# Kernel optimization log

Measured on AMD Instinct MI355X. Metric: run time of the kernel, lower is better.

## Reference

```python
import jax, jax.numpy as jnp
import numpy as np
import math

FACTOR = 5  # self.factor


def setup_inputs() -> dict:
    key = jax.random.key(0)
    kq, kk, kv = jax.random.split(key, 3)
    B, L, H, D = 4, 2048, 8, 64
    return {
        "queries": jax.random.normal(kq, (B, L, H, D), dtype=jnp.float32),
        "keys": jax.random.normal(kk, (B, L, H, D), dtype=jnp.float32),
        "values": jax.random.normal(kv, (B, L, H, D), dtype=jnp.float32),
        "attn_mask": jnp.zeros((1,), dtype=jnp.int32),  # unused by the module's forward
    }


def _prob_attention(queries, keys, values):
    B, L_Q, H, D = queries.shape
    L_K = keys.shape[1]
    # to (B, H, L, D)
    Q = queries.transpose(0, 2, 1, 3)
    K = keys.transpose(0, 2, 1, 3)
    V = values.transpose(0, 2, 1, 3)

    U_part = min(FACTOR * int(math.ceil(math.log(L_K))), L_K)  # sample_k
    u = min(FACTOR * int(math.ceil(math.log(L_Q))), L_Q)       # n_top

    # --- _prob_QE: sampled QK, sparsity measure M, top-u query selection ---
    idx_key = jax.random.key(42)  # fixed key stands in for torch.randint
    index_sample = jax.random.randint(idx_key, (L_Q, U_part), 0, L_K)  # [L_Q, S]
    K_sample = K[:, :, index_sample, :]                                # [B,H,L_Q,S,E]
    Q_K_sample = jnp.einsum('bhqe,bhqse->bhqs', Q, K_sample)           # [B,H,L_Q,S]
    M = Q_K_sample.max(axis=-1) - Q_K_sample.sum(axis=-1) / L_K        # [B,H,L_Q]
    M_top = jax.lax.top_k(M, u)[1]                                     # [B,H,u]

    Q_reduce = jnp.take_along_axis(Q, M_top[..., None], axis=2)        # [B,H,u,E]
    scores = jnp.einsum('bhue,bhke->bhuk', Q_reduce, K)                # [B,H,u,L_K]
    scores = scores * (1.0 / math.sqrt(D))                             # scale=None -> 1/sqrt(D)

    # --- initial context (mask_flag=True path): mean of V over keys ---
    context = jnp.broadcast_to(V.mean(axis=2, keepdims=True), (B, H, L_Q, D))

    attn = jax.nn.softmax(scores, axis=-1)
    context_update = jnp.einsum('bhuk,bhkd->bhud', attn, V)            # [B,H,u,D]

    # scatter the updated rows back at the selected query positions
    b = jnp.arange(B)[:, None, None]
    h = jnp.arange(H)[None, :, None]
    context = context.at[b, h, M_top].set(context_update)

    return context.transpose(0, 2, 1, 3)  # [B, L_Q, H, D]


def reference(queries, keys, values, attn_mask):
    # attn_mask is accepted but unused by the torch module's mask_flag=True path
    return _prob_attention(queries, keys, values)
```

## Files before the change

kernel.cpp:

```cpp
#include <hip/hip_runtime.h>
#include <stdint.h>


static constexpr int Bc = 4, Lc = 2048, Hc = 8, Dc = 64, NUc = 40;
static constexpr int NCH = 32, CHK = 64;
static constexpr int UT = 10;

struct TF2 { uint32_t a, b; };

__host__ __device__ constexpr uint32_t rotl32c(uint32_t x, int r) {
    return (x << r) | (x >> (32 - r));
}

__host__ __device__ constexpr TF2 tf2x32c(uint32_t k0, uint32_t k1, uint32_t x0, uint32_t x1) {
    uint32_t ks[3] = {k0, k1, k0 ^ k1 ^ 0x1BD11BDAu};
    const int R0[4] = {13, 15, 26, 6};
    const int R1[4] = {17, 29, 16, 24};
    x0 += ks[0];
    x1 += ks[1];
    for (int i = 0; i < 5; ++i) {
        const int* R = (i & 1) ? R1 : R0;
        for (int j = 0; j < 4; ++j) {
            x0 += x1;
            x1 = rotl32c(x1, R[j]);
            x1 ^= x0;
        }
        x0 += ks[(i + 1) % 3];
        x1 += ks[(i + 2) % 3] + (uint32_t)(i + 1);
    }
    return TF2{x0, x1};
}

__global__ __launch_bounds__(256, 4) void k_M(const float* __restrict__ Q,
                                              const float* __restrict__ K,
                                              float* __restrict__ M,
                                              float* __restrict__ vm) {
    constexpr TF2 K2 = tf2x32c(0u, 42u, 0u, 1u);
    int lane = threadIdx.x & 63;
    int w = threadIdx.x >> 6;
    int blk = blockIdx.x;
    if (blk < 8) vm[blk * 256 + threadIdx.x] = 0.f;
    int xcd = blk & 7;
    int local = blk >> 3;
    int b = xcd >> 1;
    int q = (xcd & 1) * 1024 + local * 4 + w;
    int h = lane >> 3;
    int myidx = 0;
    if (lane < 40) {
        TF2 r = tf2x32c(K2.a, K2.b, 0u, (uint32_t)(q * 40 + lane));
        myidx = (int)((r.a ^ r.b) & 2047u);
    }

    const float4* Q4 = reinterpret_cast<const float4*>(Q);
    const float4* K4 = reinterpret_cast<const float4*>(K);
    size_t qb = (size_t)(b * Lc + q) * 128;
    float4 qv0 = Q4[qb + 2 * lane];
    float4 qv1 = Q4[qb + 2 * lane + 1];

    float mx8[8], sm8[8];
#pragma unroll
    for (int j = 0; j < 8; ++j) { mx8[j] = -INFINITY; sm8[j] = 0.f; }
#pragma unroll
    for (int i = 0; i < 5; ++i) {
#pragma unroll
        for (int j = 0; j < 8; ++j) {
            int kk = __shfl(myidx, i * 8 + j, 64);
            size_t rb = (size_t)(b * Lc + kk) * 128;
            float4 kv0 = K4[rb + 2 * lane];
            float4 kv1 = K4[rb + 2 * lane + 1];
            float pv = qv0.x * kv0.x + qv0.y * kv0.y + qv0.z * kv0.z + qv0.w * kv0.w +
                       qv1.x * kv1.x + qv1.y * kv1.y + qv1.z * kv1.z + qv1.w * kv1.w;
#pragma unroll
            for (int m = 1; m < 8; m <<= 1) pv += __shfl_xor(pv, m, 64);
            mx8[j] = fmaxf(mx8[j], pv);
            sm8[j] += pv;
        }
    }
    float mx = mx8[0], sm = sm8[0];
#pragma unroll
    for (int j = 1; j < 8; ++j) { mx = fmaxf(mx, mx8[j]); sm += sm8[j]; }
    if ((lane & 7) == 0) M[(b * 8 + h) * Lc + q] = mx - sm * (1.0f / 2048.0f);
}

__global__ __launch_bounds__(256) void k_topk(const float* __restrict__ M, int* __restrict__ top,
                                              uint32_t* __restrict__ gmask) {
    __shared__ uint32_t hist[256];
    __shared__ uint32_t sh_bin, sh_need;
    __shared__ int sel[NUc];
    __shared__ int tie[128];
    __shared__ uint32_t selCnt, tieCnt;
    int bh = blockIdx.x;
    int t = threadIdx.x;
    uint32_t uk[8];
#pragma unroll
    for (int i = 0; i < 8; ++i) {
        uint32_t s = __float_as_uint(M[bh * Lc + i * 256 + t]);
        uk[i] = (s & 0x80000000u) ? ~s : (s | 0x80000000u);
    }
    uint32_t prefix = 0, need = NUc;
    for (int pass = 0; pass < 4; ++pass) {
        int shift = 24 - 8 * pass;
        hist[t] = 0;
        __syncthreads();
#pragma unroll
        for (int i = 0; i < 8; ++i) {
            bool ok = (pass == 0) || ((uk[i] >> (shift + 8)) == prefix);
            if (ok) atomicAdd(&hist[(uk[i] >> shift) & 255u], 1u);
        }
        __syncthreads();
        if (t < 64) {
            uint32_t c0 = hist[4 * t], c1 = hist[4 * t + 1];
            uint32_t c2 = hist[4 * t + 2], c3 = hist[4 * t + 3];
            uint32_t s = c0 + c1 + c2 + c3;
            uint32_t suf = s;
#pragma unroll
            for (int m = 1; m < 64; m <<= 1) {
                uint32_t o = __shfl_down(suf, m, 64);
                if (t + m < 64) suf += o;
            }
            uint32_t above = suf - s;
            if (suf >= need && above < need) {
                uint32_t rem = need - above;
                uint32_t bsel, cnt;
                if (c3 >= rem) { bsel = 4 * t + 3; cnt = rem; }
                else if (c3 + c2 >= rem) { bsel = 4 * t + 2; cnt = rem - c3; }
                else if (c3 + c2 + c1 >= rem) { bsel = 4 * t + 1; cnt = rem - c3 - c2; }
                else { bsel = 4 * t; cnt = rem - c3 - c2 - c1; }
                sh_bin = bsel;
                sh_need = cnt;
            }
        }
        __syncthreads();
        prefix = (pass == 0) ? sh_bin : ((prefix << 8) | sh_bin);
        need = sh_need;
        __syncthreads();
    }
    const uint32_t T = prefix;
    if (t == 0) { selCnt = 0; tieCnt = 0; }
    __syncthreads();
#pragma unroll
    for (int i = 0; i < 8; ++i) {
        int idx = i * 256 + t;
        if (uk[i] > T) {
            uint32_t slot = atomicAdd(&selCnt, 1u);
            if (slot < NUc) sel[slot] = idx;
        } else if (uk[i] == T) {
            uint32_t slot = atomicAdd(&tieCnt, 1u);
            if (slot < 128) tie[slot] = idx;
        }
    }
    __syncthreads();
    if (t == 0) {
        int n = (int)tieCnt;
        if (n > 128) n = 128;
        for (int a = 1; a < n; ++a) {
            int key = tie[a], c = a - 1;
            while (c >= 0 && tie[c] > key) { tie[c + 1] = tie[c]; --c; }
            tie[c + 1] = key;
        }
        uint32_t base = selCnt;
        for (uint32_t j = 0; j < need && base + j < NUc; ++j) sel[base + j] = tie[j];
    }
    __syncthreads();
    if (t < NUc) top[bh * NUc + t] = sel[t];
    if (t < 64) {
        uint32_t word = 0;
#pragma unroll
        for (int j = 0; j < NUc; ++j) {
            int s = sel[j];
            if ((s >> 5) == t) word |= 1u << (s & 31);
        }
        gmask[bh * 64 + t] = word;
    }
}

__global__ __launch_bounds__(64, 4) void k_attn_part(const float* __restrict__ Q,
                                                     const float* __restrict__ K,
                                                     const float* __restrict__ V,
                                                     const int* __restrict__ top,
                                                     float* __restrict__ wsO,
                                                     float* __restrict__ wsm,
                                                     float* __restrict__ wsl,
                                                     float* __restrict__ vm) {
    __shared__ float Qs[UT][64];
    __shared__ float pT[64][12];
    __shared__ int tqs[UT];
    int blk = blockIdx.x;
    int xcd = blk & 7, local = blk >> 3;
    int bh = xcd * 4 + (local >> 7);
    int rem = local & 127;
    int chunk = rem >> 2, ut = rem & 3;
    int b = bh >> 3, h = bh & 7;
    int t = threadIdx.x;

    if (t < UT) tqs[t] = top[bh * NUc + ut * UT + t];
    __syncthreads();
#pragma unroll
    for (int j = 0; j < UT; ++j)
        Qs[j][t] = Q[(((size_t)(b * Lc + tqs[j])) * Hc + h) * Dc + t];
    __syncthreads();

    int kg = chunk * CHK + t;
    const float4* Kr = reinterpret_cast<const float4*>(&K[(((size_t)(b * Lc + kg)) * Hc + h) * Dc]);
    float acc[UT];
#pragma unroll
    for (int u = 0; u < UT; ++u) acc[u] = 0.f;
#pragma unroll
    for (int i = 0; i < 16; ++i) {
        float4 kv = Kr[i];
#pragma unroll
        for (int u = 0; u < UT; ++u) {
            float4 qv = *reinterpret_cast<const float4*>(&Qs[u][i * 4]);
            acc[u] += qv.x * kv.x + qv.y * kv.y + qv.z * kv.z + qv.w * kv.w;
        }
    }
#pragma unroll
    for (int u = 0; u < UT; ++u) acc[u] *= 0.125f;
    float mr[UT];
#pragma unroll
    for (int u = 0; u < UT; ++u) {
        float v = acc[u];
#pragma unroll
        for (int m = 1; m < 64; m <<= 1) v = fmaxf(v, __shfl_xor(v, m, 64));
        mr[u] = v;
    }
    float pr[UT];
#pragma unroll
    for (int u = 0; u < UT; ++u) {
        pr[u] = __expf(acc[u] - mr[u]);
        pT[t][u] = pr[u];
    }
    float sr[UT];
#pragma unroll
    for (int u = 0; u < UT; ++u) {
        float v = pr[u];
#pragma unroll
        for (int m = 1; m < 64; m <<= 1) v += __shfl_xor(v, m, 64);
        sr[u] = v;
    }
    int sbase = (bh * NCH + chunk) * NUc + ut * UT;
#pragma unroll
    for (int u = 0; u < UT; ++u) {
        if (t == u) {
            wsm[sbase + u] = mr[u];
            wsl[sbase + u] = sr[u];
        }
    }
    __syncthreads();
#pragma unroll
    for (int u = 0; u < UT; ++u) acc[u] = 0.f;
    float vs = 0.f;
    const float* Vbh = V + ((size_t)b * Lc * Hc + h) * Dc;
    for (int k = 0; k < 64; ++k) {
        float vv = Vbh[(size_t)(chunk * CHK + k) * 512 + t];
        vs += vv;
        float4 pa = *reinterpret_cast<const float4*>(&pT[k][0]);
        float4 pb = *reinterpret_cast<const float4*>(&pT[k][4]);
        float2 pc = *reinterpret_cast<const float2*>(&pT[k][8]);
        acc[0] += pa.x * vv; acc[1] += pa.y * vv; acc[2] += pa.z * vv; acc[3] += pa.w * vv;
        acc[4] += pb.x * vv; acc[5] += pb.y * vv; acc[6] += pb.z * vv; acc[7] += pb.w * vv;
        acc[8] += pc.x * vv; acc[9] += pc.y * vv;
    }
    if (ut == 0) atomicAdd(&vm[bh * 64 + t], vs * (1.0f / 2048.0f));
    size_t obase = (size_t)(bh * NCH + chunk) * 2560 + (size_t)(ut * UT) * 64;
#pragma unroll
    for (int u = 0; u < UT; ++u) wsO[obase + u * 64 + t] = acc[u];
}

__global__ void k_out_inl(const float* __restrict__ wsO, const float* __restrict__ wsm,
                          const float* __restrict__ wsl, const float* __restrict__ vm,
                          const int* __restrict__ top, const uint32_t* __restrict__ gmask,
                          float* __restrict__ out) {
    int o4 = blockIdx.x * blockDim.x + threadIdx.x;
    if (o4 >= Bc * Lc * Hc * (Dc / 4)) return;
    int dq = o4 & 15;
    int h = (o4 >> 4) & 7;
    int bl = o4 >> 7;
    int b = bl >> 11, l = bl & 2047;
    int bh = b * 8 + h;
    float4 v;
    uint32_t wmask = gmask[bh * 64 + (l >> 5)];
    if ((wmask >> (l & 31)) & 1u) {
        int u = 0;
#pragma unroll
        for (int j = 0; j < NUc; ++j)
            if (top[bh * NUc + j] == l) u = j;
        float cf[NCH];
        float m = -INFINITY;
#pragma unroll
        for (int c = 0; c < NCH; ++c) {
            cf[c] = wsm[(bh * NCH + c) * NUc + u];
            m = fmaxf(m, cf[c]);
        }
        float L = 0.f;
#pragma unroll
        for (int c = 0; c < NCH; ++c) {
            float e = __expf(cf[c] - m);
            L += wsl[(bh * NCH + c) * NUc + u] * e;
            cf[c] = e;
        }
        const float4* W4 = reinterpret_cast<const float4*>(wsO);
        float4 a = make_float4(0.f, 0.f, 0.f, 0.f);
#pragma unroll
        for (int c = 0; c < NCH; ++c) {
            float4 o = W4[(size_t)(bh * NCH + c) * 640 + u * 16 + dq];
            a.x += o.x * cf[c]; a.y += o.y * cf[c]; a.z += o.z * cf[c]; a.w += o.w * cf[c];
        }
        float inv = 1.0f / L;
        v = make_float4(a.x * inv, a.y * inv, a.z * inv, a.w * inv);
    } else {
        v = reinterpret_cast<const float4*>(vm)[bh * 16 + dq];
    }
    reinterpret_cast<float4*>(out)[o4] = v;
}

__global__ __launch_bounds__(256) void k_comb(const float* __restrict__ wsO,
                                              const float* __restrict__ wsm,
                                              const float* __restrict__ wsl,
                                              float* __restrict__ stage) {
    __shared__ float cm[NCH][5], cl[NCH][5], cf[NCH][5];
    int blk = blockIdx.x;
    int ut = blk & 7, bh = blk >> 3;
    int t = threadIdx.x;
    for (int i = t; i < NCH * 5; i += 256) {
        int c = i / 5, j = i % 5;
        cm[c][j] = wsm[(bh * NCH + c) * NUc + ut * 5 + j];
        cl[c][j] = wsl[(bh * NCH + c) * NUc + ut * 5 + j];
    }
    __syncthreads();
    if (t < 5) {
        float m = -INFINITY;
#pragma unroll
        for (int c = 0; c < NCH; ++c) m = fmaxf(m, cm[c][t]);
        float L = 0.f;
#pragma unroll
        for (int c = 0; c < NCH; ++c) {
            float f = __expf(cm[c][t] - m);
            L += cl[c][t] * f;
            cf[c][t] = f;
        }
        float inv = 1.0f / L;
#pragma unroll
        for (int c = 0; c < NCH; ++c) cf[c][t] *= inv;
    }
    __syncthreads();
    for (int i = t; i < 5 * 64; i += 256) {
        int j = i >> 6, d = i & 63;
        float val = 0.f;
#pragma unroll
        for (int c = 0; c < NCH; ++c)
            val += wsO[((size_t)(bh * NCH + c)) * 2560 + (ut * 5 + j) * 64 + d] * cf[c][j];
        stage[(size_t)bh * 2560 + (ut * 5 + j) * 64 + d] = val;
    }
}

__global__ void k_out(const float* __restrict__ stage, const float* __restrict__ vm,
                      const int* __restrict__ top, const uint32_t* __restrict__ gmask,
                      float* __restrict__ out) {
    int o4 = blockIdx.x * blockDim.x + threadIdx.x;
    if (o4 >= Bc * Lc * Hc * (Dc / 4)) return;
    int dq = o4 & 15;
    int h = (o4 >> 4) & 7;
    int bl = o4 >> 7;
    int b = bl >> 11, l = bl & 2047;
    int bh = b * 8 + h;
    float4 v;
    uint32_t wmask = gmask[bh * 64 + (l >> 5)];
    if ((wmask >> (l & 31)) & 1u) {
        int u = 0;
#pragma unroll
        for (int j = 0; j < NUc; ++j)
            if (top[bh * NUc + j] == l) u = j;
        v = reinterpret_cast<const float4*>(stage)[(bh * NUc + u) * 16 + dq];
    } else {
        v = reinterpret_cast<const float4*>(vm)[bh * 16 + dq];
    }
    reinterpret_cast<float4*>(out)[o4] = v;
}

extern "C" void kernel_launch(void* const* d_in, const int* in_sizes, int n_in,
                              void* d_out, int out_size, void* d_ws, size_t ws_size,
                              hipStream_t stream) {
    (void)in_sizes; (void)n_in; (void)out_size;
    const float* Q = (const float*)d_in[0];
    const float* K = (const float*)d_in[1];
    const float* V = (const float*)d_in[2];
    float* out = (float*)d_out;

    int*      top   = (int*)d_ws;
    float*    vm    = (float*)((char*)d_ws + 8192);
    uint32_t* gmask = (uint32_t*)((char*)d_ws + 16384);
    float* M = (float*)((char*)d_out + 11075584);

    const bool bigws = ws_size >= 11534336;

    if (bigws) {
        float* wsm = (float*)((char*)d_ws + 32768);
        float* wsl = (float*)((char*)d_ws + 196608);
        float* wsO = (float*)((char*)d_ws + 393216);
        hipLaunchKernelGGL(k_M, dim3(2048), dim3(256), 0, stream, Q, K, M, vm);
        hipLaunchKernelGGL(k_topk, dim3(Bc * Hc), dim3(256), 0, stream, M, top, gmask);
        hipLaunchKernelGGL(k_attn_part, dim3(4096), dim3(64), 0, stream, Q, K, V, top,
                           wsO, wsm, wsl, vm);
        hipLaunchKernelGGL(k_out_inl, dim3(4096), dim3(256), 0, stream, wsO, wsm, wsl, vm,
                           top, gmask, out);
    } else {
        float* wsO   = (float*)d_out;
        float* wsm   = (float*)((char*)d_out + 10485760);
        float* wsl   = (float*)((char*)d_out + 10649600);
        float* stage = (float*)((char*)d_ws + 24576);
        hipLaunchKernelGGL(k_M, dim3(2048), dim3(256), 0, stream, Q, K, M, vm);
        hipLaunchKernelGGL(k_topk, dim3(Bc * Hc), dim3(256), 0, stream, M, top, gmask);
        hipLaunchKernelGGL(k_attn_part, dim3(4096), dim3(64), 0, stream, Q, K, V, top,
                           wsO, wsm, wsl, vm);
        hipLaunchKernelGGL(k_comb, dim3(Bc * Hc * 8), dim3(256), 0, stream, wsO, wsm, wsl,
                           stage);
        hipLaunchKernelGGL(k_out, dim3(4096), dim3(256), 0, stream, stage, vm, top, gmask,
                           out);
    }
}
```

Measured before the change: 91.96 us.

## Merge four query-group blocks into one 256-thread block sharing a staged K chunk

Each k_attn_part block previously handled one 64-key chunk for 10 selected queries, so the same K chunk and V rows were read by four separate blocks. The block now has four wavefronts, each taking 10 queries, with the K chunk staged once in padded shared memory and all 40 Q rows loaded together. The grid shrinks from 4096 blocks to 1024, which cuts redundant global traffic for K and Q but leaves fewer blocks and more shared memory per block. V is still read separately by each wave, and the barrier before the PV loop is dropped because each wave reads only its own pT slice.

Result: no change. 90.72 us (-1.3%).

```diff
diff --git a/kernel.cpp b/kernel.cpp
--- a/kernel.cpp
+++ b/kernel.cpp
@@ -174,43 +174,48 @@
     }
 }
 
-__global__ __launch_bounds__(64, 4) void k_attn_part(const float* __restrict__ Q,
-                                                     const float* __restrict__ K,
-                                                     const float* __restrict__ V,
-                                                     const int* __restrict__ top,
-                                                     float* __restrict__ wsO,
-                                                     float* __restrict__ wsm,
-                                                     float* __restrict__ wsl,
-                                                     float* __restrict__ vm) {
-    __shared__ float Qs[UT][64];
-    __shared__ float pT[64][12];
-    __shared__ int tqs[UT];
+__global__ __launch_bounds__(256, 4) void k_attn_part(const float* __restrict__ Q,
+                                                      const float* __restrict__ K,
+                                                      const float* __restrict__ V,
+                                                      const int* __restrict__ top,
+                                                      float* __restrict__ wsO,
+                                                      float* __restrict__ wsm,
+                                                      float* __restrict__ wsl,
+                                                      float* __restrict__ vm) {
+    __shared__ float Qs[40][64];
+    __shared__ float Ks[64][68];
+    __shared__ float pT[4][64][12];
+    __shared__ int tqs[40];
     int blk = blockIdx.x;
     int xcd = blk & 7, local = blk >> 3;
-    int bh = xcd * 4 + (local >> 7);
-    int rem = local & 127;
-    int chunk = rem >> 2, ut = rem & 3;
+    int bh = xcd * 4 + (local >> 5);
+    int chunk = local & 31;
     int b = bh >> 3, h = bh & 7;
-    int t = threadIdx.x;
-
-    if (t < UT) tqs[t] = top[bh * NUc + ut * UT + t];
-    __syncthreads();
-#pragma unroll
-    for (int j = 0; j < UT; ++j)
-        Qs[j][t] = Q[(((size_t)(b * Lc + tqs[j])) * Hc + h) * Dc + t];
-    __syncthreads();
-
-    int kg = chunk * CHK + t;
-    const float4* Kr = reinterpret_cast<const float4*>(&K[(((size_t)(b * Lc + kg)) * Hc + h) * Dc]);
+    int t = threadIdx.x, w = t >> 6, lane = t & 63;
+
+    if (t < 40) tqs[t] = top[bh * NUc + t];
+    __syncthreads();
+    for (int i = t; i < 40 * 64; i += 256) {
+        int u = i >> 6, d = i & 63;
+        Qs[u][d] = Q[(((size_t)(b * Lc + tqs[u])) * Hc + h) * Dc + d];
+    }
+    const float* Kbase = K + (((size_t)(b * Lc + chunk * CHK)) * Hc + h) * Dc;
+    for (int f = t; f < 1024; f += 256) {
+        int r = f >> 4, c = f & 15;
+        *reinterpret_cast<float4*>(&Ks[r][c * 4]) =
+            *reinterpret_cast<const float4*>(Kbase + (size_t)r * 512 + c * 4);
+    }
+    __syncthreads();
+
     float acc[UT];
 #pragma unroll
     for (int u = 0; u < UT; ++u) acc[u] = 0.f;
 #pragma unroll
     for (int i = 0; i < 16; ++i) {
-        float4 kv = Kr[i];
+        float4 kv = *reinterpret_cast<const float4*>(&Ks[lane][i * 4]);
 #pragma unroll
         for (int u = 0; u < UT; ++u) {
-            float4 qv = *reinterpret_cast<const float4*>(&Qs[u][i * 4]);
+            float4 qv = *reinterpret_cast<const float4*>(&Qs[w * UT + u][i * 4]);
             acc[u] += qv.x * kv.x + qv.y * kv.y + qv.z * kv.z + qv.w * kv.w;
         }
     }
@@ -228,7 +233,7 @@
 #pragma unroll
     for (int u = 0; u < UT; ++u) {
         pr[u] = __expf(acc[u] - mr[u]);
-        pT[t][u] = pr[u];
+        pT[w][lane][u] = pr[u];
     }
     float sr[UT];
 #pragma unroll
@@ -238,33 +243,32 @@
         for (int m = 1; m < 64; m <<= 1) v += __shfl_xor(v, m, 64);
         sr[u] = v;
     }
-    int sbase = (bh * NCH + chunk) * NUc + ut * UT;
+    int sbase = (bh * NCH + chunk) * NUc + w * UT;
 #pragma unroll
     for (int u = 0; u < UT; ++u) {
-        if (t == u) {
+        if (lane == u) {
             wsm[sbase + u] = mr[u];
             wsl[sbase + u] = sr[u];
         }
     }
-    __syncthreads();
 #pragma unroll
     for (int u = 0; u < UT; ++u) acc[u] = 0.f;
     float vs = 0.f;
     const float* Vbh = V + ((size_t)b * Lc * Hc + h) * Dc;
     for (int k = 0; k < 64; ++k) {
-        float vv = Vbh[(size_t)(chunk * CHK + k) * 512 + t];
+        float vv = Vbh[(size_t)(chunk * CHK + k) * 512 + lane];
         vs += vv;
-        float4 pa = *reinterpret_cast<const float4*>(&pT[k][0]);
-        float4 pb = *reinterpret_cast<const float4*>(&pT[k][4]);
-        float2 pc = *reinterpret_cast<const float2*>(&pT[k][8]);
+        float4 pa = *reinterpret_cast<const float4*>(&pT[w][k][0]);
+        float4 pb = *reinterpret_cast<const float4*>(&pT[w][k][4]);
+        float2 pc = *reinterpret_cast<const float2*>(&pT[w][k][8]);
         acc[0] += pa.x * vv; acc[1] += pa.y * vv; acc[2] += pa.z * vv; acc[3] += pa.w * vv;
         acc[4] += pb.x * vv; acc[5] += pb.y * vv; acc[6] += pb.z * vv; acc[7] += pb.w * vv;
         acc[8] += pc.x * vv; acc[9] += pc.y * vv;
     }
-    if (ut == 0) atomicAdd(&vm[bh * 64 + t], vs * (1.0f / 2048.0f));
-    size_t obase = (size_t)(bh * NCH + chunk) * 2560 + (size_t)(ut * UT) * 64;
-#pragma unroll
-    for (int u = 0; u < UT; ++u) wsO[obase + u * 64 + t] = acc[u];
+    if (w == 0) atomicAdd(&vm[bh * 64 + lane], vs * (1.0f / 2048.0f));
+    size_t obase = (size_t)(bh * NCH + chunk) * 2560 + (size_t)(w * UT) * 64;
+#pragma unroll
+    for (int u = 0; u < UT; ++u) wsO[obase + u * 64 + lane] = acc[u];
 }
 
 __global__ void k_out_inl(const float* __restrict__ wsO, const float* __restrict__ wsm,
@@ -400,7 +404,7 @@
         float* wsO = (float*)((char*)d_ws + 393216);
         hipLaunchKernelGGL(k_M, dim3(2048), dim3(256), 0, stream, Q, K, M, vm);
         hipLaunchKernelGGL(k_topk, dim3(Bc * Hc), dim3(256), 0, stream, M, top, gmask);
-        hipLaunchKernelGGL(k_attn_part, dim3(4096), dim3(64), 0, stream, Q, K, V, top,
+        hipLaunchKernelGGL(k_attn_part, dim3(1024), dim3(256), 0, stream, Q, K, V, top,
                            wsO, wsm, wsl, vm);
         hipLaunchKernelGGL(k_out_inl, dim3(4096), dim3(256), 0, stream, wsO, wsm, wsl, vm,
                            top, gmask, out);
@@ -411,7 +415,7 @@
         float* stage = (float*)((char*)d_ws + 24576);
         hipLaunchKernelGGL(k_M, dim3(2048), dim3(256), 0, stream, Q, K, M, vm);
         hipLaunchKernelGGL(k_topk, dim3(Bc * Hc), dim3(256), 0, stream, M, top, gmask);
-        hipLaunchKernelGGL(k_attn_part, dim3(4096), dim3(64), 0, stream, Q, K, V, top,
+        hipLaunchKernelGGL(k_attn_part, dim3(1024), dim3(256), 0, stream, Q, K, V, top,
                            wsO, wsm, wsl, vm);
         hipLaunchKernelGGL(k_comb, dim3(Bc * Hc * 8), dim3(256), 0, stream, wsO, wsm, wsl,
                            stage);
```
